# Kernel tuning notes

Measured on AMD Instinct MI355X. Metric: run time of the kernel, lower is better.

The kernel has to match this reference:

```python
import jax, jax.numpy as jnp
import numpy as np

N_NODES = 50000
N_EDGES = 800000
IN_CH, HID_CH, OUT_CH = 128, 128, 64


def setup_inputs() -> dict:
    key = jax.random.key(0)
    ks = jax.random.split(key, 8)
    x = jax.random.normal(ks[0], (N_NODES, IN_CH), dtype=jnp.float32)
    edge_index = jax.random.randint(ks[1], (2, N_EDGES), 0, N_NODES, dtype=jnp.int64)
    # PyG SAGEConv params: lin_l (applied to aggregated neighbors, has bias),
    # lin_r (applied to root node, no bias). Stored here as [in, out] matrices.
    s1 = 1.0 / np.sqrt(IN_CH)
    s2 = 1.0 / np.sqrt(HID_CH)
    W1l = jax.random.uniform(ks[2], (IN_CH, HID_CH), jnp.float32, -s1, s1)
    b1 = jnp.zeros((HID_CH,), jnp.float32)
    W1r = jax.random.uniform(ks[3], (IN_CH, HID_CH), jnp.float32, -s1, s1)
    W2l = jax.random.uniform(ks[4], (HID_CH, OUT_CH), jnp.float32, -s2, s2)
    b2 = jnp.zeros((OUT_CH,), jnp.float32)
    W2r = jax.random.uniform(ks[5], (HID_CH, OUT_CH), jnp.float32, -s2, s2)
    return {"x": x, "edge_index": edge_index, "W1l": W1l, "b1": b1,
            "W1r": W1r, "W2l": W2l, "b2": b2, "W2r": W2r}


def _sage_conv(x, src, dst, Wl, b, Wr):
    # mean-aggregate source features onto targets, then linear transform
    msg = x[src]                                        # [E, d] gather
    agg = jax.ops.segment_sum(msg, dst, num_segments=N_NODES)   # [N, d]
    deg = jax.ops.segment_sum(jnp.ones((src.shape[0],), x.dtype), dst,
                              num_segments=N_NODES)     # [N]
    mean = agg / jnp.maximum(deg, 1.0)[:, None]
    return mean @ Wl + b + x @ Wr


def reference(x, edge_index, W1l, b1, W1r, W2l, b2, W2r):
    src, dst = edge_index[0], edge_index[1]
    h = jax.nn.relu(_sage_conv(x, src, dst, W1l, b1, W1r))
    # F.dropout(p=0.3) is identity in eval mode
    return _sage_conv(h, src, dst, W2l, b2, W2r)
```

## Files before the change

kernel.cpp:

```cpp
#include <hip/hip_runtime.h>
#include <hip/hip_bf16.h>


#define TBLOCK 256
#define MAXBUCK 1024
#define HGRID 512

typedef __attribute__((ext_vector_type(8))) short short8;
typedef __attribute__((ext_vector_type(4))) float f32x4;

__device__ __forceinline__ float bf2f(ushort u) {
    union { unsigned int i; float f; } v;
    v.i = (unsigned int)u << 16;
    return v.f;
}
__device__ __forceinline__ ushort f2bf(float f) {
    union { float f; unsigned int u; } v;
    v.f = f;
    unsigned int r = v.u + 0x7fffu + ((v.u >> 16) & 1u);
    return (ushort)(r >> 16);
}

__device__ __forceinline__ int block_detect_is64(const int* __restrict__ edges) {
    __shared__ int sbad[4];
    int tid = threadIdx.x;
    int bad = 0;
    for (int i = tid; i < 2048; i += TBLOCK)
        if (edges[2 * i + 1] != 0) bad = 1;
    unsigned long long b = __ballot(bad);
    if ((tid & 63) == 0) sbad[tid >> 6] = (b != 0) ? 1 : 0;
    __syncthreads();
    int flag = (sbad[0] | sbad[1] | sbad[2] | sbad[3]) ? 0 : 1;
    __syncthreads();
    return flag;
}

__device__ __forceinline__ int load_src(const int* e, long long i, int E, int is64) {
    return is64 ? e[2 * i] : e[i];
}
__device__ __forceinline__ int load_dst(const int* e, long long i, int E, int is64) {
    return is64 ? e[2 * (long long)E + 2 * i] : e[(long long)E + i];
}

__global__ __launch_bounds__(TBLOCK) void histprep_k(
    const float* __restrict__ x,
    const float* __restrict__ W1l, const float* __restrict__ W1r,
    const float* __restrict__ W2l, const float* __restrict__ W2r,
    const int* __restrict__ edges, int E, int NBUCK,
    ushort* __restrict__ xb, ushort* __restrict__ wc1, ushort* __restrict__ wc2,
    int* __restrict__ counts, int n8, int nxb) {
    __shared__ int lh[MAXBUCK];
    const int b = blockIdx.x;
    const int t = threadIdx.x;
    if (b < HGRID) {
        const int is64 = block_detect_is64(edges);
        for (int i = t; i < NBUCK; i += TBLOCK) lh[i] = 0;
        __syncthreads();
        const int per = (E + HGRID - 1) / HGRID;
        const int b0 = b * per, b1 = min(E, b0 + per);
        for (int i = b0 + t; i < b1; i += TBLOCK)
            atomicAdd(&lh[load_dst(edges, i, E, is64) >> 8], 1);
        __syncthreads();
        for (int j = t; j < NBUCK; j += TBLOCK)
            counts[j * HGRID + b] = lh[j];
    } else {
        int pb = b - HGRID;
        if (pb < nxb) {
            int i = pb * TBLOCK + t;
            if (i >= n8) return;
            const float4* p = (const float4*)x + (size_t)i * 2;
            float4 a = p[0], bb = p[1];
            short8 o;
            o[0] = f2bf(a.x); o[1] = f2bf(a.y); o[2] = f2bf(a.z); o[3] = f2bf(a.w);
            o[4] = f2bf(bb.x); o[5] = f2bf(bb.y); o[6] = f2bf(bb.z); o[7] = f2bf(bb.w);
            *(short8*)(xb + (size_t)i * 8) = o;
        } else {
            int i = (pb - nxb) * TBLOCK + t;
            if (i < 32768) {
                int j = i & 7;
                int rest = i >> 3;
                int n = rest & 127;
                int k = ((rest >> 7) << 3) | j;
                float w = (k < 128) ? W1l[k * 128 + n] : W1r[(k - 128) * 128 + n];
                wc1[i] = f2bf(w);
            } else if (i < 49152) {
                int i2 = i - 32768;
                int j = i2 & 7;
                int rest = i2 >> 3;
                int n = rest & 127;
                int k = ((rest >> 7) << 3) | j;
                float w = (n < 64) ? W2l[k * 64 + n] : W2r[k * 64 + (n - 64)];
                wc2[i2] = f2bf(w);
            }
        }
    }
}

__global__ __launch_bounds__(TBLOCK) void scanA_k(int* __restrict__ counts,
                                                  int* __restrict__ total) {
    __shared__ int s[TBLOCK];
    const int j = blockIdx.x;
    const int t = threadIdx.x;
    int* row = counts + (size_t)j * HGRID;
    int v0 = row[2 * t];
    int v1 = row[2 * t + 1];
    s[t] = v0 + v1;
    __syncthreads();
    for (int off = 1; off < TBLOCK; off <<= 1) {
        int xv = (t >= off) ? s[t - off] : 0;
        __syncthreads();
        s[t] += xv;
        __syncthreads();
    }
    int excl = (t == 0) ? 0 : s[t - 1];
    row[2 * t] = excl;
    row[2 * t + 1] = excl + v0;
    if (t == TBLOCK - 1) total[j] = s[t];
}

__global__ __launch_bounds__(TBLOCK) void scanB_k(const int* __restrict__ total,
                                                  int* __restrict__ baseg, int NBUCK) {
    __shared__ int s[TBLOCK];
    const int t = threadIdx.x;
    int v = (t < NBUCK) ? total[t] : 0;
    s[t] = v;
    __syncthreads();
    for (int off = 1; off < TBLOCK; off <<= 1) {
        int xv = (t >= off) ? s[t - off] : 0;
        __syncthreads();
        s[t] += xv;
        __syncthreads();
    }
    if (t < NBUCK) {
        baseg[t] = (t == 0) ? 0 : s[t - 1];
        if (t == NBUCK - 1) baseg[NBUCK] = s[t];
    }
}

__global__ __launch_bounds__(TBLOCK) void scatterA_k(const int* __restrict__ edges, int E,
                                                     const int* __restrict__ counts,
                                                     const int* __restrict__ baseg,
                                                     unsigned int* __restrict__ packed,
                                                     int NBUCK) {
    const int is64 = block_detect_is64(edges);
    __shared__ int lb[MAXBUCK];
    __shared__ int lh[MAXBUCK];
    const int b = blockIdx.x;
    const int t = threadIdx.x;
    for (int j = t; j < NBUCK; j += TBLOCK) {
        lb[j] = baseg[j] + counts[j * HGRID + b];
        lh[j] = 0;
    }
    __syncthreads();
    const int per = (E + HGRID - 1) / HGRID;
    const int b0 = b * per, b1 = min(E, b0 + per);
    for (int i = b0 + t; i < b1; i += TBLOCK) {
        int s = load_src(edges, i, E, is64);
        int d = load_dst(edges, i, E, is64);
        int bk = d >> 8;
        int pos = lb[bk] + atomicAdd(&lh[bk], 1);
        packed[pos] = (unsigned int)s | ((unsigned int)(d & 255) << 24);
    }
}

__global__ __launch_bounds__(TBLOCK) void buildB_k(const unsigned int* __restrict__ packed,
                                                   const int* __restrict__ baseg,
                                                   int* __restrict__ offs,
                                                   int* __restrict__ degi,
                                                   float* __restrict__ invdeg,
                                                   int* __restrict__ csr, int N) {
    __shared__ int cnt[TBLOCK], scn[TBLOCK], cur[TBLOCK];
    int t = threadIdx.x;
    int bucket = blockIdx.x;
    int e0 = baseg[bucket], e1 = baseg[bucket + 1];
    cnt[t] = 0;
    cur[t] = 0;
    __syncthreads();
    for (int i = e0 + t; i < e1; i += TBLOCK)
        atomicAdd(&cnt[packed[i] >> 24], 1);
    __syncthreads();
    scn[t] = cnt[t];
    __syncthreads();
    for (int off = 1; off < TBLOCK; off <<= 1) {
        int x = (t >= off) ? scn[t - off] : 0;
        __syncthreads();
        scn[t] += x;
        __syncthreads();
    }
    int excl = (t == 0) ? 0 : scn[t - 1];
    int node = bucket * 256 + t;
    if (node < N) {
        offs[node] = e0 + excl;
        degi[node] = cnt[t];
        invdeg[node] = 1.0f / fmaxf((float)cnt[t], 1.0f);
    }
    __syncthreads();
    cnt[t] = excl;
    __syncthreads();
    for (int i = e0 + t; i < e1; i += TBLOCK) {
        unsigned int p = packed[i];
        int nl = p >> 24;
        int pos = e0 + cnt[nl] + atomicAdd(&cur[nl], 1);
        csr[pos] = (int)(p & 0xFFFFFFu);
    }
}

template <int C, bool ACCUM>
__global__ __launch_bounds__(TBLOCK) void gatherb_k(const ushort* __restrict__ feat,
                                                    const int* __restrict__ csr,
                                                    const int* __restrict__ offs,
                                                    const int* __restrict__ degi,
                                                    const float* __restrict__ invdeg,
                                                    ushort* __restrict__ outB,
                                                    float* __restrict__ outF, int N) {
    constexpr int G = C / 8;
    constexpr int NPB = TBLOCK / G;
    int n = blockIdx.x * NPB + threadIdx.x / G;
    if (n >= N) return;
    int lane = threadIdx.x % G;
    int c = lane * 8;
    int s0 = offs[n];
    int d = degi[n];
    float acc[8] = {0.f, 0.f, 0.f, 0.f, 0.f, 0.f, 0.f, 0.f};
    for (int base = 0; base < d; base += G) {
        int rem = d - base;
        int my = (lane < rem) ? csr[s0 + base + lane] : 0;
        if (rem >= G) {
#pragma unroll
            for (int j = 0; j < G; j++) {
                int s = __shfl(my, j, G);
                short8 v = *(const short8*)(feat + (size_t)s * C + c);
#pragma unroll
                for (int q = 0; q < 8; q++) acc[q] += bf2f((ushort)v[q]);
            }
        } else {
            for (int j = 0; j < rem; j++) {
                int s = __shfl(my, j, G);
                short8 v = *(const short8*)(feat + (size_t)s * C + c);
#pragma unroll
                for (int q = 0; q < 8; q++) acc[q] += bf2f((ushort)v[q]);
            }
        }
    }
    float sc = invdeg[n];
    if (ACCUM) {
        float* o = outF + (size_t)n * C + c;
        float4 p0 = *(float4*)o;
        float4 p1 = *(float4*)(o + 4);
        p0.x += sc * acc[0]; p0.y += sc * acc[1]; p0.z += sc * acc[2]; p0.w += sc * acc[3];
        p1.x += sc * acc[4]; p1.y += sc * acc[5]; p1.z += sc * acc[6]; p1.w += sc * acc[7];
        *(float4*)o = p0;
        *(float4*)(o + 4) = p1;
    } else {
        short8 o;
#pragma unroll
        for (int q = 0; q < 8; q++) o[q] = f2bf(sc * acc[q]);
        *(short8*)(outB + (size_t)n * C + c) = o;
    }
}

template <int KTOT, int EPI>
__global__ __launch_bounds__(TBLOCK) void gemm_k(const ushort* __restrict__ A0,
                                                 const ushort* __restrict__ A1,
                                                 const ushort* __restrict__ wc,
                                                 const float* __restrict__ bias,
                                                 ushort* __restrict__ outB,
                                                 float* __restrict__ outF, int N) {
    __shared__ __align__(16) ushort sW[KTOT * 128];
    for (int i = threadIdx.x * 8; i < KTOT * 128; i += TBLOCK * 8)
        *(short8*)&sW[i] = *(const short8*)&wc[i];
    __syncthreads();

    const int wave = threadIdx.x >> 6;
    const int lane = threadIdx.x & 63;
    const int quad = lane >> 4;
    const int l16 = lane & 15;
    const int m0 = (blockIdx.x * 4 + wave) * 32;
    if (m0 >= N) return;

    f32x4 acc[2][8];
#pragma unroll
    for (int t = 0; t < 2; t++)
#pragma unroll
        for (int nt = 0; nt < 8; nt++) acc[t][nt] = (f32x4){0.f, 0.f, 0.f, 0.f};

    const int k0q = quad * 8;
#pragma unroll
    for (int kb = 0; kb < KTOT; kb += 32) {
        int k = kb + k0q;
        const ushort* abase = (KTOT == 256 && k >= 128) ? (A1 + (k - 128)) : (A0 + k);
        short8 a[2];
#pragma unroll
        for (int t = 0; t < 2; t++) {
            int m = m0 + t * 16 + l16;
            if (m > N - 1) m = N - 1;
            a[t] = *(const short8*)(abase + (size_t)m * 128);
        }
#pragma unroll
        for (int nt = 0; nt < 8; nt++) {
            short8 b = *(const short8*)&sW[((k >> 3) * 128 + nt * 16 + l16) * 8];
            acc[0][nt] = __builtin_amdgcn_mfma_f32_16x16x32_bf16(a[0], b, acc[0][nt], 0, 0, 0);
            acc[1][nt] = __builtin_amdgcn_mfma_f32_16x16x32_bf16(a[1], b, acc[1][nt], 0, 0, 0);
        }
    }

#pragma unroll
    for (int t = 0; t < 2; t++) {
#pragma unroll
        for (int r = 0; r < 4; r++) {
            int m = m0 + t * 16 + quad * 4 + r;
            if (m >= N) continue;
#pragma unroll
            for (int nt = 0; nt < 8; nt++) {
                int n = nt * 16 + l16;
                float v = acc[t][nt][r];
                if (EPI == 1) {
                    v = fmaxf(v + bias[n], 0.f);
                    outB[(size_t)m * 128 + n] = f2bf(v);
                } else {
                    if (n < 64) outB[(size_t)m * 64 + n] = f2bf(v);
                    else outF[(size_t)m * 64 + (n - 64)] = v + bias[n - 64];
                }
            }
        }
    }
}

extern "C" void kernel_launch(void* const* d_in, const int* in_sizes, int n_in,
                              void* d_out, int out_size, void* d_ws, size_t ws_size,
                              hipStream_t stream) {
    const float* x = (const float*)d_in[0];
    const int* edges = (const int*)d_in[1];
    const float* W1l = (const float*)d_in[2];
    const float* b1 = (const float*)d_in[3];
    const float* W1r = (const float*)d_in[4];
    const float* W2l = (const float*)d_in[5];
    const float* b2 = (const float*)d_in[6];
    const float* W2r = (const float*)d_in[7];
    float* out = (float*)d_out;

    const int N = in_sizes[0] / 128;
    const int E = in_sizes[1] / 2;
    const int Na = (N + 63) & ~63;
    const int NBUCK = (N + 255) >> 8;
    const int n8 = N * 128 / 8;
    const int nxb = (n8 + TBLOCK - 1) / TBLOCK;

    char* WS = (char*)d_ws;
    size_t off = 0;
    auto alloc = [&](size_t bytes) {
        void* p = WS + off;
        off = (off + bytes + 255) & ~(size_t)255;
        return p;
    };
    int* counts = (int*)alloc((size_t)MAXBUCK * HGRID * 4);
    int* total = (int*)alloc((size_t)MAXBUCK * 4);
    int* baseg = (int*)alloc((size_t)(MAXBUCK + 1) * 4);
    int* offs = (int*)alloc((size_t)Na * 4);
    int* degi = (int*)alloc((size_t)Na * 4);
    float* invdeg = (float*)alloc((size_t)Na * 4);
    unsigned int* packed = (unsigned int*)alloc((size_t)E * 4);
    int* csr = (int*)alloc((size_t)E * 4);
    ushort* xb = (ushort*)alloc((size_t)N * 128 * 2);
    ushort* agg1b = (ushort*)alloc((size_t)N * 128 * 2);
    ushort* hb = (ushort*)alloc((size_t)N * 128 * 2);
    ushort* t2b = (ushort*)alloc((size_t)N * 64 * 2);
    ushort* wc1 = (ushort*)alloc(32768 * 2);
    ushort* wc2 = (ushort*)alloc(16384 * 2);

    histprep_k<<<HGRID + nxb + 192, TBLOCK, 0, stream>>>(
        x, W1l, W1r, W2l, W2r, edges, E, NBUCK, xb, wc1, wc2, counts, n8, nxb);
    scanA_k<<<NBUCK, TBLOCK, 0, stream>>>(counts, total);
    scanB_k<<<1, TBLOCK, 0, stream>>>(total, baseg, NBUCK);
    scatterA_k<<<HGRID, TBLOCK, 0, stream>>>(edges, E, counts, baseg, packed, NBUCK);
    buildB_k<<<NBUCK, TBLOCK, 0, stream>>>(packed, baseg, offs, degi, invdeg, csr, N);

    gatherb_k<128, false><<<(N + 15) / 16, TBLOCK, 0, stream>>>(
        xb, csr, offs, degi, invdeg, agg1b, nullptr, N);
    gemm_k<256, 1><<<(N + 127) / 128, TBLOCK, 0, stream>>>(
        agg1b, xb, wc1, b1, hb, nullptr, N);

    gemm_k<128, 2><<<(N + 127) / 128, TBLOCK, 0, stream>>>(
        hb, nullptr, wc2, b2, t2b, out, N);
    gatherb_k<64, true><<<(N + 31) / 32, TBLOCK, 0, stream>>>(
        t2b, csr, offs, degi, invdeg, nullptr, out, N);
}
```

Measured before the change: 194.2 us.

## Fuse two GEMMs via LDS hidden tile and fold bucket scan into consumers

Replaces the two separate GEMM launches with one kernel that computes the layer-1 hidden tile, applies bias and ReLU, stores it in padded LDS, then runs the layer-2 GEMM from LDS. This removes the global round trip of the hidden activations and one launch. It also drops the single-block scanB kernel: scatterA and buildB each recompute the bucket prefix scan from totals, and MAXBUCK shrinks to 256. Weights are now read directly from global memory instead of being staged in LDS. The smaller MAXBUCK caps node count at 65536, and the early-exit guard for out-of-range row tiles was removed.

```diff
diff --git a/kernel.cpp b/kernel.cpp
--- a/kernel.cpp
+++ b/kernel.cpp
@@ -3,7 +3,7 @@
 
 
 #define TBLOCK 256
-#define MAXBUCK 1024
+#define MAXBUCK 256
 #define HGRID 512
 
 typedef __attribute__((ext_vector_type(8))) short short8;
@@ -40,6 +40,19 @@
 }
 __device__ __forceinline__ int load_dst(const int* e, long long i, int E, int is64) {
     return is64 ? e[2 * (long long)E + 2 * i] : e[(long long)E + i];
+}
+
+__device__ __forceinline__ void scan_total(const int* __restrict__ total, int NBUCK,
+                                           int* __restrict__ s) {
+    int t = threadIdx.x;
+    s[t] = (t < NBUCK) ? total[t] : 0;
+    __syncthreads();
+    for (int off = 1; off < TBLOCK; off <<= 1) {
+        int xv = (t >= off) ? s[t - off] : 0;
+        __syncthreads();
+        s[t] += xv;
+        __syncthreads();
+    }
 }
 
 __global__ __launch_bounds__(TBLOCK) void histprep_k(
@@ -118,61 +131,48 @@
     if (t == TBLOCK - 1) total[j] = s[t];
 }
 
-__global__ __launch_bounds__(TBLOCK) void scanB_k(const int* __restrict__ total,
-                                                  int* __restrict__ baseg, int NBUCK) {
-    __shared__ int s[TBLOCK];
-    const int t = threadIdx.x;
-    int v = (t < NBUCK) ? total[t] : 0;
-    s[t] = v;
-    __syncthreads();
-    for (int off = 1; off < TBLOCK; off <<= 1) {
-        int xv = (t >= off) ? s[t - off] : 0;
-        __syncthreads();
-        s[t] += xv;
-        __syncthreads();
-    }
-    if (t < NBUCK) {
-        baseg[t] = (t == 0) ? 0 : s[t - 1];
-        if (t == NBUCK - 1) baseg[NBUCK] = s[t];
-    }
-}
-
 __global__ __launch_bounds__(TBLOCK) void scatterA_k(const int* __restrict__ edges, int E,
                                                      const int* __restrict__ counts,
-                                                     const int* __restrict__ baseg,
+                                                     const int* __restrict__ total,
                                                      unsigned int* __restrict__ packed,
                                                      int NBUCK) {
     const int is64 = block_detect_is64(edges);
+    __shared__ int s[TBLOCK];
     __shared__ int lb[MAXBUCK];
     __shared__ int lh[MAXBUCK];
     const int b = blockIdx.x;
     const int t = threadIdx.x;
-    for (int j = t; j < NBUCK; j += TBLOCK) {
-        lb[j] = baseg[j] + counts[j * HGRID + b];
-        lh[j] = 0;
+    scan_total(total, NBUCK, s);
+    if (t < NBUCK) {
+        int excl = (t == 0) ? 0 : s[t - 1];
+        lb[t] = excl + counts[t * HGRID + b];
+        lh[t] = 0;
     }
     __syncthreads();
     const int per = (E + HGRID - 1) / HGRID;
     const int b0 = b * per, b1 = min(E, b0 + per);
     for (int i = b0 + t; i < b1; i += TBLOCK) {
-        int s = load_src(edges, i, E, is64);
+        int sv = load_src(edges, i, E, is64);
         int d = load_dst(edges, i, E, is64);
         int bk = d >> 8;
         int pos = lb[bk] + atomicAdd(&lh[bk], 1);
-        packed[pos] = (unsigned int)s | ((unsigned int)(d & 255) << 24);
+        packed[pos] = (unsigned int)sv | ((unsigned int)(d & 255) << 24);
     }
 }
 
 __global__ __launch_bounds__(TBLOCK) void buildB_k(const unsigned int* __restrict__ packed,
-                                                   const int* __restrict__ baseg,
+                                                   const int* __restrict__ total,
                                                    int* __restrict__ offs,
                                                    int* __restrict__ degi,
                                                    float* __restrict__ invdeg,
-                                                   int* __restrict__ csr, int N) {
+                                                   int* __restrict__ csr, int N, int NBUCK) {
+    __shared__ int s[TBLOCK];
     __shared__ int cnt[TBLOCK], scn[TBLOCK], cur[TBLOCK];
     int t = threadIdx.x;
     int bucket = blockIdx.x;
-    int e0 = baseg[bucket], e1 = baseg[bucket + 1];
+    scan_total(total, NBUCK, s);
+    int e0 = (bucket == 0) ? 0 : s[bucket - 1];
+    int e1 = s[bucket];
     cnt[t] = 0;
     cur[t] = 0;
     __syncthreads();
@@ -259,36 +259,32 @@
     }
 }
 
-template <int KTOT, int EPI>
-__global__ __launch_bounds__(TBLOCK) void gemm_k(const ushort* __restrict__ A0,
-                                                 const ushort* __restrict__ A1,
-                                                 const ushort* __restrict__ wc,
-                                                 const float* __restrict__ bias,
-                                                 ushort* __restrict__ outB,
-                                                 float* __restrict__ outF, int N) {
-    __shared__ __align__(16) ushort sW[KTOT * 128];
-    for (int i = threadIdx.x * 8; i < KTOT * 128; i += TBLOCK * 8)
-        *(short8*)&sW[i] = *(const short8*)&wc[i];
-    __syncthreads();
-
+#define HPAD 136
+__global__ __launch_bounds__(TBLOCK) void gemmF_k(const ushort* __restrict__ agg1b,
+                                                  const ushort* __restrict__ xb,
+                                                  const ushort* __restrict__ wc1,
+                                                  const ushort* __restrict__ wc2,
+                                                  const float* __restrict__ b1,
+                                                  const float* __restrict__ b2,
+                                                  ushort* __restrict__ t2b,
+                                                  float* __restrict__ outF, int N) {
+    __shared__ __align__(16) ushort hbt[128 * HPAD];
     const int wave = threadIdx.x >> 6;
     const int lane = threadIdx.x & 63;
     const int quad = lane >> 4;
     const int l16 = lane & 15;
-    const int m0 = (blockIdx.x * 4 + wave) * 32;
-    if (m0 >= N) return;
+    const int m0 = blockIdx.x * 128 + wave * 32;
+    const int k0q = quad * 8;
 
     f32x4 acc[2][8];
 #pragma unroll
     for (int t = 0; t < 2; t++)
 #pragma unroll
         for (int nt = 0; nt < 8; nt++) acc[t][nt] = (f32x4){0.f, 0.f, 0.f, 0.f};
-
-    const int k0q = quad * 8;
-#pragma unroll
-    for (int kb = 0; kb < KTOT; kb += 32) {
+#pragma unroll
+    for (int kb = 0; kb < 256; kb += 32) {
         int k = kb + k0q;
-        const ushort* abase = (KTOT == 256 && k >= 128) ? (A1 + (k - 128)) : (A0 + k);
+        const ushort* abase = (k >= 128) ? (xb + (k - 128)) : (agg1b + k);
         short8 a[2];
 #pragma unroll
         for (int t = 0; t < 2; t++) {
@@ -298,14 +294,45 @@
         }
 #pragma unroll
         for (int nt = 0; nt < 8; nt++) {
-            short8 b = *(const short8*)&sW[((k >> 3) * 128 + nt * 16 + l16) * 8];
+            short8 b = *(const short8*)&wc1[((size_t)(k >> 3) * 128 + nt * 16 + l16) * 8];
             acc[0][nt] = __builtin_amdgcn_mfma_f32_16x16x32_bf16(a[0], b, acc[0][nt], 0, 0, 0);
             acc[1][nt] = __builtin_amdgcn_mfma_f32_16x16x32_bf16(a[1], b, acc[1][nt], 0, 0, 0);
         }
     }
-
-#pragma unroll
-    for (int t = 0; t < 2; t++) {
+#pragma unroll
+    for (int nt = 0; nt < 8; nt++) {
+        float bb = b1[nt * 16 + l16];
+#pragma unroll
+        for (int t = 0; t < 2; t++)
+#pragma unroll
+            for (int r = 0; r < 4; r++) {
+                int ml = wave * 32 + t * 16 + quad * 4 + r;
+                hbt[ml * HPAD + nt * 16 + l16] = f2bf(fmaxf(acc[t][nt][r] + bb, 0.f));
+            }
+    }
+    __syncthreads();
+
+    f32x4 acc2[2][8];
+#pragma unroll
+    for (int t = 0; t < 2; t++)
+#pragma unroll
+        for (int nt = 0; nt < 8; nt++) acc2[t][nt] = (f32x4){0.f, 0.f, 0.f, 0.f};
+#pragma unroll
+    for (int kb = 0; kb < 128; kb += 32) {
+        int k = kb + k0q;
+        short8 a[2];
+#pragma unroll
+        for (int t = 0; t < 2; t++)
+            a[t] = *(const short8*)&hbt[(wave * 32 + t * 16 + l16) * HPAD + k];
+#pragma unroll
+        for (int nt = 0; nt < 8; nt++) {
+            short8 b = *(const short8*)&wc2[((size_t)(k >> 3) * 128 + nt * 16 + l16) * 8];
+            acc2[0][nt] = __builtin_amdgcn_mfma_f32_16x16x32_bf16(a[0], b, acc2[0][nt], 0, 0, 0);
+            acc2[1][nt] = __builtin_amdgcn_mfma_f32_16x16x32_bf16(a[1], b, acc2[1][nt], 0, 0, 0);
+        }
+    }
+#pragma unroll
+    for (int t = 0; t < 2; t++)
 #pragma unroll
         for (int r = 0; r < 4; r++) {
             int m = m0 + t * 16 + quad * 4 + r;
@@ -313,17 +340,11 @@
 #pragma unroll
             for (int nt = 0; nt < 8; nt++) {
                 int n = nt * 16 + l16;
-                float v = acc[t][nt][r];
-                if (EPI == 1) {
-                    v = fmaxf(v + bias[n], 0.f);
-                    outB[(size_t)m * 128 + n] = f2bf(v);
-                } else {
-                    if (n < 64) outB[(size_t)m * 64 + n] = f2bf(v);
-                    else outF[(size_t)m * 64 + (n - 64)] = v + bias[n - 64];
-                }
+                float v = acc2[t][nt][r];
+                if (n < 64) t2b[(size_t)m * 64 + n] = f2bf(v);
+                else outF[(size_t)m * 64 + (n - 64)] = v + b2[n - 64];
             }
         }
-    }
 }
 
 extern "C" void kernel_launch(void* const* d_in, const int* in_sizes, int n_in,
@@ -355,7 +376,6 @@
     };
     int* counts = (int*)alloc((size_t)MAXBUCK * HGRID * 4);
     int* total = (int*)alloc((size_t)MAXBUCK * 4);
-    int* baseg = (int*)alloc((size_t)(MAXBUCK + 1) * 4);
     int* offs = (int*)alloc((size_t)Na * 4);
     int* degi = (int*)alloc((size_t)Na * 4);
     float* invdeg = (float*)alloc((size_t)Na * 4);
@@ -363,7 +383,6 @@
     int* csr = (int*)alloc((size_t)E * 4);
     ushort* xb = (ushort*)alloc((size_t)N * 128 * 2);
     ushort* agg1b = (ushort*)alloc((size_t)N * 128 * 2);
-    ushort* hb = (ushort*)alloc((size_t)N * 128 * 2);
     ushort* t2b = (ushort*)alloc((size_t)N * 64 * 2);
     ushort* wc1 = (ushort*)alloc(32768 * 2);
     ushort* wc2 = (ushort*)alloc(16384 * 2);
@@ -371,17 +390,13 @@
     histprep_k<<<HGRID + nxb + 192, TBLOCK, 0, stream>>>(
         x, W1l, W1r, W2l, W2r, edges, E, NBUCK, xb, wc1, wc2, counts, n8, nxb);
     scanA_k<<<NBUCK, TBLOCK, 0, stream>>>(counts, total);
-    scanB_k<<<1, TBLOCK, 0, stream>>>(total, baseg, NBUCK);
-    scatterA_k<<<HGRID, TBLOCK, 0, stream>>>(edges, E, counts, baseg, packed, NBUCK);
-    buildB_k<<<NBUCK, TBLOCK, 0, stream>>>(packed, baseg, offs, degi, invdeg, csr, N);
+    scatterA_k<<<HGRID, TBLOCK, 0, stream>>>(edges, E, counts, total, packed, NBUCK);
+    buildB_k<<<NBUCK, TBLOCK, 0, stream>>>(packed, total, offs, degi, invdeg, csr, N, NBUCK);
 
     gatherb_k<128, false><<<(N + 15) / 16, TBLOCK, 0, stream>>>(
         xb, csr, offs, degi, invdeg, agg1b, nullptr, N);
-    gemm_k<256, 1><<<(N + 127) / 128, TBLOCK, 0, stream>>>(
-        agg1b, xb, wc1, b1, hb, nullptr, N);
-
-    gemm_k<128, 2><<<(N + 127) / 128, TBLOCK, 0, stream>>>(
-        hb, nullptr, wc2, b2, t2b, out, N);
+    gemmF_k<<<(N + 127) / 128, TBLOCK, 0, stream>>>(
+        agg1b, xb, wc1, wc2, b1, b2, t2b, out, N);
     gatherb_k<64, true><<<(N + 31) / 32, TBLOCK, 0, stream>>>(
         t2b, csr, offs, degi, invdeg, nullptr, out, N);
 }
```

New measurement: 199.7 us. +2.8%, slower.
